# Performance work log

Measured on AMD Instinct MI355X. Metric: run time of the kernel, lower is better.

## Reference

```python
import jax, jax.numpy as jnp
import numpy as np

ALPHA = 0.2          # LeakyReLU negative slope
NEG_INF = -9e15      # mask value from the torch code
B, N, F, E, H, S, T, L = 32, 128, 78, 12, 256, 20, 13, 3


def setup_inputs() -> dict:
    key = jax.random.key(0)
    ks = jax.random.split(key, 20)
    sc = 0.05  # param scale
    inp = {
        "node_features": jax.random.normal(ks[0], (B, N, F), jnp.float32),
        "edge_features": jax.random.normal(ks[1], (B, N, N, E), jnp.float32),
        "adj_matrix": jax.random.randint(ks[2], (B, N, N), 0, 2).astype(jnp.int32),
        "scaffold_features": jax.random.normal(ks[3], (B, S), jnp.float32),
        # node projection (Linear F->H, with bias)
        "W_node": jax.random.normal(ks[4], (F, H), jnp.float32) * sc,
        "b_node": jnp.zeros((H,), jnp.float32),
        # stacked GAT layer params: W (H->H, no bias), a (2H->1, no bias)
        "gat_W": jax.random.normal(ks[5], (L, H, H), jnp.float32) * sc,
        "gat_a": jax.random.normal(ks[6], (L, 2 * H), jnp.float32) * sc,
        # scaffold projection (S->H)
        "W_sc": jax.random.normal(ks[7], (S, H), jnp.float32) * sc,
        "b_sc": jnp.zeros((H,), jnp.float32),
        # graph_pooling MLP: H -> H/2 -> H/4 (shared for graph + scaffold paths)
        "gp_w1": jax.random.normal(ks[8], (H, H // 2), jnp.float32) * sc,
        "gp_b1": jnp.zeros((H // 2,), jnp.float32),
        "gp_w2": jax.random.normal(ks[9], (H // 2, H // 4), jnp.float32) * sc,
        "gp_b2": jnp.zeros((H // 4,), jnp.float32),
        # output MLP: (H/4 + H/4) -> H/2 -> T
        "out_w1": jax.random.normal(ks[10], (H // 2, H // 2), jnp.float32) * sc,
        "out_b1": jnp.zeros((H // 2,), jnp.float32),
        "out_w2": jax.random.normal(ks[11], (H // 2, T), jnp.float32) * sc,
        "out_b2": jnp.zeros((T,), jnp.float32),
    }
    return inp


def _gat_stack(x, adj_matrix, gat_W, gat_a):
    # x: (B,N,H); adj: (B,N,N) int
    mask = adj_matrix > 0
    n_layers, _, h_dim = gat_W.shape
    for l in range(n_layers):
        h = jnp.einsum("bnf,fh->bnh", x, gat_W[l])      # (B,N,H)
        a1, a2 = gat_a[l, :h_dim], gat_a[l, h_dim:]
        # a . [h_i ; h_j] == h_i.a1 + h_j.a2 (exact decomposition of the
        # O(N^2, 2H) concat in the torch code)
        s1 = h @ a1                                       # (B,N)
        s2 = h @ a2                                       # (B,N)
        e = jax.nn.leaky_relu(s1[:, :, None] + s2[:, None, :], ALPHA)
        att = jnp.where(mask, e, NEG_INF)                 # (B,N,N)
        att = jax.nn.softmax(att, axis=-1)
        h_prime = jnp.einsum("bij,bjh->bih", att, h)
        x = jax.nn.relu(h_prime)                          # relu after layer (dropout = identity, eval)
    return x


def _pool(z, gp_w1, gp_b1, gp_w2, gp_b2):
    z = jax.nn.relu(z @ gp_w1 + gp_b1)
    return jax.nn.relu(z @ gp_w2 + gp_b2)


def reference(node_features, edge_features, adj_matrix, scaffold_features,
              W_node, b_node, gat_W, gat_a, W_sc, b_sc,
              gp_w1, gp_b1, gp_w2, gp_b2, out_w1, out_b1, out_w2, out_b2):
    # edge_features is accepted but unused in the original forward
    x = node_features @ W_node + b_node                  # (B,N,H)
    x = _gat_stack(x, adj_matrix, gat_W, gat_a)
    graph = x.mean(axis=1)                               # (B,H)
    g = _pool(graph, gp_w1, gp_b1, gp_w2, gp_b2)         # (B,H/4)
    s = _pool(scaffold_features @ W_sc + b_sc, gp_w1, gp_b1, gp_w2, gp_b2)
    c = jnp.concatenate([g, s], axis=-1)                 # (B,H/2)
    hdn = jax.nn.relu(c @ out_w1 + out_b1)
    return hdn @ out_w2 + out_b2                         # (B,T)
```

## Files before the change

kernel.cpp:

```cpp
#include <hip/hip_runtime.h>
#include <hip/hip_bf16.h>

#define NEG_INF -9.0e15f

using u16 = unsigned short;

__device__ __forceinline__ float b2f(__hip_bfloat16 v) { return __bfloat162float(v); }
__device__ __forceinline__ float ldv(const float* p, int i) { return p[i]; }
__device__ __forceinline__ float ldv(const __hip_bfloat16* p, int i) { return __bfloat162float(p[i]); }

__device__ __forceinline__ void async16(const void* g, void* l) {
    __builtin_amdgcn_global_load_lds(
        (__attribute__((address_space(1))) void*)(g),
        (__attribute__((address_space(3))) void*)(l), 16, 0, 0);
}

__device__ __forceinline__ int sniff(const void* wnode) {
    const u16* w = (const u16*)wnode;
    int lane = threadIdx.x & 63;
    u16 u = w[2 * lane];
    int e = (u >> 7) & 0xFF;
    unsigned long long m = __ballot(e >= 100 && e <= 140);
    return __popcll(m) >= 48;
}

__global__ __launch_bounds__(256) void k_gat(
    const float* __restrict__ x, const void* __restrict__ gat_W,
    const void* __restrict__ gat_a, int layer,
    const void* __restrict__ nf, const void* __restrict__ Wn_raw,
    const void* __restrict__ bn, int first,
    float* __restrict__ h, float* __restrict__ s1, float* __restrict__ s2) {
    __shared__ float xsT[256 * 10];
    __shared__ u16 Wbuf[2][32 * 256];
    const int t = threadIdx.x;
    const int bx = blockIdx.x;
    const int row0 = bx * 8;
    const int tx = t & 63, w = t >> 6;
    const int isbf = sniff(Wn_raw);
    const int c0 = 4 * tx;

    float acc0[4], acc1[4];

    if (isbf) {
        const u16* Wl = (const u16*)gat_W + (size_t)layer * 65536;

        auto stage_rows = [&](const u16* src, int r0, int nr, int b) {
            const char* g = (const char*)src + (size_t)r0 * 512;
            char* l = (char*)&Wbuf[b][0];
            int bytes = nr * 512;
            for (int off = t * 16; off < bytes; off += 4096)
                async16(g + off, l + off);
        };
        auto tile_compute = [&](int b, int k0, int nr) {
            const u16* Wb = &Wbuf[b][0];
            #pragma unroll 8
            for (int kk = 0; kk < nr; ++kk) {
                uint2 wv = *(const uint2*)(Wb + kk * 256 + c0);
                float w0 = __uint_as_float(wv.x << 16);
                float w1 = __uint_as_float(wv.x & 0xffff0000u);
                float w2 = __uint_as_float(wv.y << 16);
                float w3 = __uint_as_float(wv.y & 0xffff0000u);
                float2 xp = *(const float2*)&xsT[(k0 + kk) * 10 + 2 * w];
                acc0[0] += xp.x * w0; acc0[1] += xp.x * w1;
                acc0[2] += xp.x * w2; acc0[3] += xp.x * w3;
                acc1[0] += xp.y * w0; acc1[1] += xp.y * w1;
                acc1[2] += xp.y * w2; acc1[3] += xp.y * w3;
            }
        };

        int pb;
        if (first) {
            const u16* Wnl = (const u16*)Wn_raw;
            stage_rows(Wnl, 0, 32, 0);
            const u16* nfu = (const u16*)nf;
            for (int i = t; i < 624; i += 256) {
                int r = i / 78, k = i - r * 78;
                xsT[k * 10 + r] = __uint_as_float(((unsigned)nfu[(row0 + r) * 78 + k]) << 16);
            }
            const __hip_bfloat16* bnb = (const __hip_bfloat16*)bn;
            #pragma unroll
            for (int j = 0; j < 4; ++j) { acc0[j] = b2f(bnb[c0 + j]); acc1[j] = acc0[j]; }
            __syncthreads();
            stage_rows(Wnl, 32, 32, 1);
            tile_compute(0, 0, 32);
            __syncthreads();
            stage_rows(Wnl, 64, 14, 0);
            tile_compute(1, 32, 32);
            __syncthreads();
            stage_rows(Wl, 0, 32, 1);
            tile_compute(0, 64, 14);
            __syncthreads();
            #pragma unroll
            for (int j = 0; j < 4; ++j) {
                xsT[(c0 + j) * 10 + 2 * w]     = acc0[j];
                xsT[(c0 + j) * 10 + 2 * w + 1] = acc1[j];
            }
            __syncthreads();
            pb = 1;
        } else {
            stage_rows(Wl, 0, 32, 0);
            int r = t >> 5, cb = (t & 31) * 8;
            const float4* xp = (const float4*)(x + (size_t)(row0 + r) * 256 + cb);
            float4 f0 = xp[0], f1 = xp[1];
            xsT[(cb + 0) * 10 + r] = f0.x; xsT[(cb + 1) * 10 + r] = f0.y;
            xsT[(cb + 2) * 10 + r] = f0.z; xsT[(cb + 3) * 10 + r] = f0.w;
            xsT[(cb + 4) * 10 + r] = f1.x; xsT[(cb + 5) * 10 + r] = f1.y;
            xsT[(cb + 6) * 10 + r] = f1.z; xsT[(cb + 7) * 10 + r] = f1.w;
            __syncthreads();
            pb = 0;
        }
        #pragma unroll
        for (int j = 0; j < 4; ++j) { acc0[j] = 0.f; acc1[j] = 0.f; }
        for (int tt = 0; tt < 8; ++tt) {
            if (tt < 7) stage_rows(Wl, 32 * (tt + 1), 32, pb ^ 1);
            tile_compute(pb, 32 * tt, 32);
            __syncthreads();
            pb ^= 1;
        }
        const __hip_bfloat16* ga = (const __hip_bfloat16*)gat_a + (size_t)layer * 512;
        float d10 = 0.f, d20 = 0.f, d11 = 0.f, d21 = 0.f;
        #pragma unroll
        for (int j = 0; j < 4; ++j) {
            float a1v = b2f(ga[c0 + j]), a2v = b2f(ga[256 + c0 + j]);
            d10 += acc0[j] * a1v; d20 += acc0[j] * a2v;
            d11 += acc1[j] * a1v; d21 += acc1[j] * a2v;
        }
        #pragma unroll
        for (int off = 1; off < 64; off <<= 1) {
            d10 += __shfl_xor(d10, off, 64); d20 += __shfl_xor(d20, off, 64);
            d11 += __shfl_xor(d11, off, 64); d21 += __shfl_xor(d21, off, 64);
        }
        if (tx == 0) {
            s1[row0 + 2 * w] = d10;     s2[row0 + 2 * w] = d20;
            s1[row0 + 2 * w + 1] = d11; s2[row0 + 2 * w + 1] = d21;
        }
        *(float4*)&h[(size_t)(row0 + 2 * w) * 256 + c0]     = (float4){acc0[0], acc0[1], acc0[2], acc0[3]};
        *(float4*)&h[(size_t)(row0 + 2 * w + 1) * 256 + c0] = (float4){acc1[0], acc1[1], acc1[2], acc1[3]};
    } else {
        const float* Wlf = (const float*)gat_W + (size_t)layer * 65536;
        const float* gaf = (const float*)gat_a + (size_t)layer * 512;
        if (first) {
            const float* nff = (const float*)nf;
            for (int i = t; i < 624; i += 256) {
                int r = i / 78, k = i - r * 78;
                xsT[k * 10 + r] = nff[(row0 + r) * 78 + k];
            }
            __syncthreads();
            const float* Wnf = (const float*)Wn_raw;
            const float* bnf = (const float*)bn;
            #pragma unroll
            for (int j = 0; j < 4; ++j) { acc0[j] = bnf[c0 + j]; acc1[j] = acc0[j]; }
            for (int k = 0; k < 78; ++k) {
                float4 wf = *(const float4*)(Wnf + k * 256 + c0);
                float2 xp = *(const float2*)&xsT[k * 10 + 2 * w];
                acc0[0] += xp.x * wf.x; acc0[1] += xp.x * wf.y;
                acc0[2] += xp.x * wf.z; acc0[3] += xp.x * wf.w;
                acc1[0] += xp.y * wf.x; acc1[1] += xp.y * wf.y;
                acc1[2] += xp.y * wf.z; acc1[3] += xp.y * wf.w;
            }
            __syncthreads();
            #pragma unroll
            for (int j = 0; j < 4; ++j) {
                xsT[(c0 + j) * 10 + 2 * w]     = acc0[j];
                xsT[(c0 + j) * 10 + 2 * w + 1] = acc1[j];
            }
            __syncthreads();
        } else {
            int r = t >> 5, cb = (t & 31) * 8;
            const float4* xp = (const float4*)(x + (size_t)(row0 + r) * 256 + cb);
            float4 f0 = xp[0], f1 = xp[1];
            xsT[(cb + 0) * 10 + r] = f0.x; xsT[(cb + 1) * 10 + r] = f0.y;
            xsT[(cb + 2) * 10 + r] = f0.z; xsT[(cb + 3) * 10 + r] = f0.w;
            xsT[(cb + 4) * 10 + r] = f1.x; xsT[(cb + 5) * 10 + r] = f1.y;
            xsT[(cb + 6) * 10 + r] = f1.z; xsT[(cb + 7) * 10 + r] = f1.w;
            __syncthreads();
        }
        #pragma unroll
        for (int j = 0; j < 4; ++j) { acc0[j] = 0.f; acc1[j] = 0.f; }
        #pragma unroll 4
        for (int k = 0; k < 256; ++k) {
            float4 wf = *(const float4*)(Wlf + k * 256 + c0);
            float2 xp = *(const float2*)&xsT[k * 10 + 2 * w];
            acc0[0] += xp.x * wf.x; acc0[1] += xp.x * wf.y;
            acc0[2] += xp.x * wf.z; acc0[3] += xp.x * wf.w;
            acc1[0] += xp.y * wf.x; acc1[1] += xp.y * wf.y;
            acc1[2] += xp.y * wf.z; acc1[3] += xp.y * wf.w;
        }
        float d10 = 0.f, d20 = 0.f, d11 = 0.f, d21 = 0.f;
        #pragma unroll
        for (int j = 0; j < 4; ++j) {
            float a1v = gaf[c0 + j], a2v = gaf[256 + c0 + j];
            d10 += acc0[j] * a1v; d20 += acc0[j] * a2v;
            d11 += acc1[j] * a1v; d21 += acc1[j] * a2v;
        }
        #pragma unroll
        for (int off = 1; off < 64; off <<= 1) {
            d10 += __shfl_xor(d10, off, 64); d20 += __shfl_xor(d20, off, 64);
            d11 += __shfl_xor(d11, off, 64); d21 += __shfl_xor(d21, off, 64);
        }
        if (tx == 0) {
            s1[row0 + 2 * w] = d10;     s2[row0 + 2 * w] = d20;
            s1[row0 + 2 * w + 1] = d11; s2[row0 + 2 * w + 1] = d21;
        }
        *(float4*)&h[(size_t)(row0 + 2 * w) * 256 + c0]     = (float4){acc0[0], acc0[1], acc0[2], acc0[3]};
        *(float4*)&h[(size_t)(row0 + 2 * w + 1) * 256 + c0] = (float4){acc1[0], acc1[1], acc1[2], acc1[3]};
    }
}

__global__ __launch_bounds__(256) void k_attn(
    const float* __restrict__ h, const float* __restrict__ s1,
    const float* __restrict__ s2, const int* __restrict__ adj,
    float* __restrict__ x, float* __restrict__ gpart, int do_pool) {
    __shared__ float att_t[128][10];
    __shared__ __align__(16) float hbuf[2][32 * 256];
    __shared__ float pool_red[4][256];
    int blk = blockIdx.x, b = blk >> 4, i0 = (blk & 15) << 3;
    int t = threadIdx.x, w = t >> 6, lane = t & 63;
    const char* hbytes = (const char*)(h + (size_t)b * 32768);
    const int ph = blk & 3;
    {
        char* lb = (char*)&hbuf[0][0];
        const char* g = hbytes + ph * 32768;
        #pragma unroll
        for (int i = 0; i < 8; ++i)
            async16(g + i * 4096 + t * 16, lb + i * 4096 + t * 16);
    }
    {
        int cc0 = lane, cc1 = lane + 64;
        int ir0 = i0 + 2 * w, ir1 = ir0 + 1;
        const int* a0 = adj + (size_t)(b * 128 + ir0) * 128;
        const int* a1 = adj + (size_t)(b * 128 + ir1) * 128;
        int m00 = a0[cc0], m01 = a0[cc1], m10 = a1[cc0], m11 = a1[cc1];
        float sv0 = s1[b * 128 + ir0], sv1 = s1[b * 128 + ir1];
        float t0 = s2[b * 128 + cc0],  t1 = s2[b * 128 + cc1];
        float e00 = sv0 + t0; e00 = (e00 >= 0.f) ? e00 : 0.2f * e00;
        float e01 = sv0 + t1; e01 = (e01 >= 0.f) ? e01 : 0.2f * e01;
        float e10 = sv1 + t0; e10 = (e10 >= 0.f) ? e10 : 0.2f * e10;
        float e11 = sv1 + t1; e11 = (e11 >= 0.f) ? e11 : 0.2f * e11;
        float v00 = (m00 > 0) ? e00 : NEG_INF;
        float v01 = (m01 > 0) ? e01 : NEG_INF;
        float v10 = (m10 > 0) ? e10 : NEG_INF;
        float v11 = (m11 > 0) ? e11 : NEG_INF;
        float mx0 = fmaxf(v00, v01), mx1 = fmaxf(v10, v11);
        #pragma unroll
        for (int off = 1; off < 64; off <<= 1) {
            mx0 = fmaxf(mx0, __shfl_xor(mx0, off, 64));
            mx1 = fmaxf(mx1, __shfl_xor(mx1, off, 64));
        }
        float p00 = __expf(v00 - mx0), p01 = __expf(v01 - mx0);
        float p10 = __expf(v10 - mx1), p11 = __expf(v11 - mx1);
        float s0 = p00 + p01, ss1 = p10 + p11;
        #pragma unroll
        for (int off = 1; off < 64; off <<= 1) {
            s0  += __shfl_xor(s0, off, 64);
            ss1 += __shfl_xor(ss1, off, 64);
        }
        float inv0 = 1.0f / s0, inv1 = 1.0f / ss1;
        att_t[cc0][2 * w]     = p00 * inv0;
        att_t[cc1][2 * w]     = p01 * inv0;
        att_t[cc0][2 * w + 1] = p10 * inv1;
        att_t[cc1][2 * w + 1] = p11 * inv1;
    }
    __syncthreads();
    int tx = t & 63, ty = t >> 6;
    float acc0[4] = {0.f, 0.f, 0.f, 0.f}, acc1[4] = {0.f, 0.f, 0.f, 0.f};
    for (int c = 0; c < 4; ++c) {
        if (c < 3) {
            char* lb = (char*)&hbuf[(c + 1) & 1][0];
            const char* g = hbytes + (((c + 1 + ph) & 3) * 32768);
            #pragma unroll
            for (int i = 0; i < 8; ++i)
                async16(g + i * 4096 + t * 16, lb + i * 4096 + t * 16);
        }
        const float* hc = &hbuf[c & 1][0];
        const int jb = ((c + ph) & 3) * 32;
        #pragma unroll 4
        for (int jj = 0; jj < 32; ++jj) {
            float4 hv = *(const float4*)&hc[jj * 256 + 4 * tx];
            float2 ap = *(const float2*)&att_t[jb + jj][2 * ty];
            acc0[0] += ap.x * hv.x; acc0[1] += ap.x * hv.y;
            acc0[2] += ap.x * hv.z; acc0[3] += ap.x * hv.w;
            acc1[0] += ap.y * hv.x; acc1[1] += ap.y * hv.y;
            acc1[2] += ap.y * hv.z; acc1[3] += ap.y * hv.w;
        }
        __syncthreads();
    }
    if (!do_pool) {
        float4 o0 = {fmaxf(acc0[0],0.f), fmaxf(acc0[1],0.f), fmaxf(acc0[2],0.f), fmaxf(acc0[3],0.f)};
        float4 o1 = {fmaxf(acc1[0],0.f), fmaxf(acc1[1],0.f), fmaxf(acc1[2],0.f), fmaxf(acc1[3],0.f)};
        *(float4*)&x[(size_t)(b * 128 + i0 + 2 * ty)     * 256 + 4 * tx] = o0;
        *(float4*)&x[(size_t)(b * 128 + i0 + 2 * ty + 1) * 256 + 4 * tx] = o1;
    } else {
        float4 pr = {(fmaxf(acc0[0],0.f) + fmaxf(acc1[0],0.f)) * (1.f/128.f),
                     (fmaxf(acc0[1],0.f) + fmaxf(acc1[1],0.f)) * (1.f/128.f),
                     (fmaxf(acc0[2],0.f) + fmaxf(acc1[2],0.f)) * (1.f/128.f),
                     (fmaxf(acc0[3],0.f) + fmaxf(acc1[3],0.f)) * (1.f/128.f)};
        *(float4*)&pool_red[ty][4 * tx] = pr;
        __syncthreads();
        if (t < 64) {
            float4 r0 = ((const float4*)&pool_red[0][0])[t];
            float4 r1 = ((const float4*)&pool_red[1][0])[t];
            float4 r2 = ((const float4*)&pool_red[2][0])[t];
            float4 r3 = ((const float4*)&pool_red[3][0])[t];
            float4 o = {r0.x+r1.x+r2.x+r3.x, r0.y+r1.y+r2.y+r3.y,
                        r0.z+r1.z+r2.z+r3.z, r0.w+r1.w+r2.w+r3.w};
            *(float4*)&gpart[((size_t)b * 16 + (blk & 15)) * 256 + 4 * t] = o;
        }
    }
}

template <typename T>
__device__ __forceinline__ void head_body(
    int b, int t, const float* __restrict__ gpart,
    const T* scaf, const T* W_sc, const T* b_sc,
    const T* gp_w1, const T* gp_b1, const T* gp_w2, const T* gp_b2,
    const T* out_w1, const T* out_b1, const T* out_w2, const T* out_b2,
    float* gin_s, float* sproj, float* scaf_s,
    float* red1, float* red2, float* z1g, float* z1s,
    float* cvec, float* hdn, float* outv) {
    float g = 0.f;
    #pragma unroll
    for (int gg = 0; gg < 16; ++gg) g += gpart[((size_t)b * 16 + gg) * 256 + t];
    gin_s[t] = g;
    if (t < 20) scaf_s[t] = ldv(scaf, b * 20 + t);
    __syncthreads();
    {
        float sa = ldv(b_sc, t);
        #pragma unroll
        for (int k = 0; k < 20; ++k) sa += scaf_s[k] * ldv(W_sc, k * 256 + t);
        sproj[t] = sa;
    }
    __syncthreads();
    {
        int j = t & 127, khalf = t >> 7;
        int k0 = khalf * 128;
        float a1 = 0.f, a2 = 0.f;
        #pragma unroll 16
        for (int kk = 0; kk < 128; ++kk) {
            int k = k0 + kk;
            float wv = ldv(gp_w1, k * 128 + j);
            a1 += gin_s[k] * wv;
            a2 += sproj[k] * wv;
        }
        red1[t] = a1; red2[t] = a2;
    }
    __syncthreads();
    if (t < 128) {
        float bb = ldv(gp_b1, t);
        z1g[t] = fmaxf(bb + red1[t] + red1[t + 128], 0.f);
        z1s[t] = fmaxf(bb + red2[t] + red2[t + 128], 0.f);
    }
    __syncthreads();
    {
        int j = t & 63, q = t >> 6;
        int k0 = q * 32;
        float a1 = 0.f, a2 = 0.f;
        #pragma unroll
        for (int kk = 0; kk < 32; ++kk) {
            int k = k0 + kk;
            float wv = ldv(gp_w2, k * 64 + j);
            a1 += z1g[k] * wv;
            a2 += z1s[k] * wv;
        }
        red1[t] = a1; red2[t] = a2;
    }
    __syncthreads();
    if (t < 64) {
        float bb = ldv(gp_b2, t);
        cvec[t]      = fmaxf(bb + red1[t] + red1[t + 64] + red1[t + 128] + red1[t + 192], 0.f);
        cvec[64 + t] = fmaxf(bb + red2[t] + red2[t + 64] + red2[t + 128] + red2[t + 192], 0.f);
    }
    __syncthreads();
    {
        int j = t & 127, khalf = t >> 7;
        int k0 = khalf * 64;
        float a = 0.f;
        #pragma unroll 16
        for (int kk = 0; kk < 64; ++kk) {
            int k = k0 + kk;
            a += cvec[k] * ldv(out_w1, k * 128 + j);
        }
        red1[t] = a;
    }
    __syncthreads();
    if (t < 128) hdn[t] = fmaxf(ldv(out_b1, t) + red1[t] + red1[t + 128], 0.f);
    __syncthreads();
    if (t < 13) {
        float a = ldv(out_b2, t);
        #pragma unroll 16
        for (int k = 0; k < 128; ++k) a += hdn[k] * ldv(out_w2, k * 13 + t);
        outv[t] = a;
    }
}

__global__ __launch_bounds__(256) void k_head(
    const float* __restrict__ gpart, const void* __restrict__ scaf,
    const void* __restrict__ W_sc, const void* __restrict__ b_sc,
    const void* __restrict__ gp_w1, const void* __restrict__ gp_b1,
    const void* __restrict__ gp_w2, const void* __restrict__ gp_b2,
    const void* __restrict__ out_w1, const void* __restrict__ out_b1,
    const void* __restrict__ out_w2, const void* __restrict__ out_b2,
    void* __restrict__ out, const void* __restrict__ Wn) {
    int isbf = sniff(Wn);
    int b = blockIdx.x;
    int t = threadIdx.x;
    __shared__ float gin_s[256], sproj[256], scaf_s[20];
    __shared__ float red1[256], red2[256];
    __shared__ float z1g[128], z1s[128], cvec[128], hdn[128], outv[13];
    if (isbf) {
        head_body<__hip_bfloat16>(b, t, gpart,
            (const __hip_bfloat16*)scaf, (const __hip_bfloat16*)W_sc, (const __hip_bfloat16*)b_sc,
            (const __hip_bfloat16*)gp_w1, (const __hip_bfloat16*)gp_b1,
            (const __hip_bfloat16*)gp_w2, (const __hip_bfloat16*)gp_b2,
            (const __hip_bfloat16*)out_w1, (const __hip_bfloat16*)out_b1,
            (const __hip_bfloat16*)out_w2, (const __hip_bfloat16*)out_b2,
            gin_s, sproj, scaf_s, red1, red2, z1g, z1s, cvec, hdn, outv);
    } else {
        head_body<float>(b, t, gpart,
            (const float*)scaf, (const float*)W_sc, (const float*)b_sc,
            (const float*)gp_w1, (const float*)gp_b1,
            (const float*)gp_w2, (const float*)gp_b2,
            (const float*)out_w1, (const float*)out_b1,
            (const float*)out_w2, (const float*)out_b2,
            gin_s, sproj, scaf_s, red1, red2, z1g, z1s, cvec, hdn, outv);
    }
    __syncthreads();
    if (t < 13) {
        if (isbf) ((__hip_bfloat16*)out)[b * 13 + t] = __float2bfloat16(outv[t]);
        else      ((float*)out)[b * 13 + t] = outv[t];
    }
}

extern "C" void kernel_launch(void* const* d_in, const int* in_sizes, int n_in,
                              void* d_out, int out_size, void* d_ws, size_t ws_size,
                              hipStream_t stream) {
    (void)in_sizes; (void)n_in; (void)out_size; (void)ws_size;
    const void* nf     = d_in[0];
    const int*  adj    = (const int*)d_in[2];
    const void* scaf   = d_in[3];
    const void* W_node = d_in[4];
    const void* b_node = d_in[5];
    const void* gat_W  = d_in[6];
    const void* gat_a  = d_in[7];
    const void* W_sc   = d_in[8];
    const void* b_sc   = d_in[9];
    const void* gp_w1  = d_in[10];
    const void* gp_b1  = d_in[11];
    const void* gp_w2  = d_in[12];
    const void* gp_b2  = d_in[13];
    const void* out_w1 = d_in[14];
    const void* out_b1 = d_in[15];
    const void* out_w2 = d_in[16];
    const void* out_b2 = d_in[17];

    float* ws    = (float*)d_ws;
    float* x     = ws;
    float* h     = ws + 1048576;
    float* s1    = ws + 2097152;
    float* s2    = s1 + 4096;
    float* gpart = s2 + 4096;

    for (int l = 0; l < 3; ++l) {
        k_gat<<<512, 256, 0, stream>>>(x, gat_W, gat_a, l,
                                       nf, W_node, b_node, (l == 0) ? 1 : 0,
                                       h, s1, s2);
        k_attn<<<512, 256, 0, stream>>>(h, s1, s2, adj, x, gpart, (l == 2) ? 1 : 0);
    }
    k_head<<<32, 256, 0, stream>>>(gpart, scaf, W_sc, b_sc, gp_w1, gp_b1, gp_w2, gp_b2,
                                   out_w1, out_b1, out_w2, out_b2, d_out, W_node);
}
```

Baseline: 223.9 us.

## Fuse GAT layers, attention and head into one cooperative persistent kernel

Replaces the seven separate kernel launches (three projection, three attention, one head) with a single cooperative kernel that uses grid-wide syncs between stages. The h and s1/s2 buffers are double-buffered so one layer's attention reads cannot collide with the next layer's writes. Blocks are remapped so each block produces the same x rows it later consumes, which avoids one grid sync per layer. This targets launch gaps and per-kernel ramp-up, at the cost of grid-barrier latency and of only 32 blocks doing work in the head stage. A fallback to the old multi-launch path is kept in case the cooperative launch fails.

```diff
diff --git a/kernel.cpp b/kernel.cpp
--- a/kernel.cpp
+++ b/kernel.cpp
@@ -1,8 +1,10 @@
 #include <hip/hip_runtime.h>
 #include <hip/hip_bf16.h>
+#include <hip/hip_cooperative_groups.h>
 
 #define NEG_INF -9.0e15f
 
+namespace cg = cooperative_groups;
 using u16 = unsigned short;
 
 __device__ __forceinline__ float b2f(__hip_bfloat16 v) { return __bfloat162float(v); }
@@ -24,38 +26,35 @@
     return __popcll(m) >= 48;
 }
 
-__global__ __launch_bounds__(256) void k_gat(
+
+template <int IS_BF>
+__device__ __forceinline__ void gat_body(
+    char* smem, int t, int row0, int l, int first,
     const float* __restrict__ x, const void* __restrict__ gat_W,
-    const void* __restrict__ gat_a, int layer,
+    const void* __restrict__ gat_a,
     const void* __restrict__ nf, const void* __restrict__ Wn_raw,
-    const void* __restrict__ bn, int first,
-    float* __restrict__ h, float* __restrict__ s1, float* __restrict__ s2) {
-    __shared__ float xsT[256 * 10];
-    __shared__ u16 Wbuf[2][32 * 256];
-    const int t = threadIdx.x;
-    const int bx = blockIdx.x;
-    const int row0 = bx * 8;
+    const void* __restrict__ bn,
+    float* __restrict__ hw, float* __restrict__ s1w, float* __restrict__ s2w) {
+    float* xsT = (float*)smem;
     const int tx = t & 63, w = t >> 6;
-    const int isbf = sniff(Wn_raw);
     const int c0 = 4 * tx;
-
     float acc0[4], acc1[4];
 
-    if (isbf) {
-        const u16* Wl = (const u16*)gat_W + (size_t)layer * 65536;
-
-        auto stage_rows = [&](const u16* src, int r0, int nr, int b) {
+    if (IS_BF) {
+        u16* Wb0 = (u16*)(smem + 10240);
+        const u16* Wl = (const u16*)gat_W + (size_t)l * 65536;
+        auto stage_rows = [&](const u16* src, int r0, int nr, int buf) {
             const char* g = (const char*)src + (size_t)r0 * 512;
-            char* l = (char*)&Wbuf[b][0];
+            char* lp = (char*)(Wb0 + buf * 8192);
             int bytes = nr * 512;
             for (int off = t * 16; off < bytes; off += 4096)
-                async16(g + off, l + off);
+                async16(g + off, lp + off);
         };
-        auto tile_compute = [&](int b, int k0, int nr) {
-            const u16* Wb = &Wbuf[b][0];
+        auto tile_compute = [&](int buf, int k0, int nr) {
+            const u16* Wp = Wb0 + buf * 8192;
             #pragma unroll 8
             for (int kk = 0; kk < nr; ++kk) {
-                uint2 wv = *(const uint2*)(Wb + kk * 256 + c0);
+                uint2 wv = *(const uint2*)(Wp + kk * 256 + c0);
                 float w0 = __uint_as_float(wv.x << 16);
                 float w1 = __uint_as_float(wv.x & 0xffff0000u);
                 float w2 = __uint_as_float(wv.y << 16);
@@ -67,7 +66,6 @@
                 acc1[2] += xp.y * w2; acc1[3] += xp.y * w3;
             }
         };
-
         int pb;
         if (first) {
             const u16* Wnl = (const u16*)Wn_raw;
@@ -117,7 +115,7 @@
             __syncthreads();
             pb ^= 1;
         }
-        const __hip_bfloat16* ga = (const __hip_bfloat16*)gat_a + (size_t)layer * 512;
+        const __hip_bfloat16* ga = (const __hip_bfloat16*)gat_a + (size_t)l * 512;
         float d10 = 0.f, d20 = 0.f, d11 = 0.f, d21 = 0.f;
         #pragma unroll
         for (int j = 0; j < 4; ++j) {
@@ -131,14 +129,14 @@
             d11 += __shfl_xor(d11, off, 64); d21 += __shfl_xor(d21, off, 64);
         }
         if (tx == 0) {
-            s1[row0 + 2 * w] = d10;     s2[row0 + 2 * w] = d20;
-            s1[row0 + 2 * w + 1] = d11; s2[row0 + 2 * w + 1] = d21;
-        }
-        *(float4*)&h[(size_t)(row0 + 2 * w) * 256 + c0]     = (float4){acc0[0], acc0[1], acc0[2], acc0[3]};
-        *(float4*)&h[(size_t)(row0 + 2 * w + 1) * 256 + c0] = (float4){acc1[0], acc1[1], acc1[2], acc1[3]};
+            s1w[row0 + 2 * w] = d10;     s2w[row0 + 2 * w] = d20;
+            s1w[row0 + 2 * w + 1] = d11; s2w[row0 + 2 * w + 1] = d21;
+        }
+        *(float4*)&hw[(size_t)(row0 + 2 * w) * 256 + c0]     = (float4){acc0[0], acc0[1], acc0[2], acc0[3]};
+        *(float4*)&hw[(size_t)(row0 + 2 * w + 1) * 256 + c0] = (float4){acc1[0], acc1[1], acc1[2], acc1[3]};
     } else {
-        const float* Wlf = (const float*)gat_W + (size_t)layer * 65536;
-        const float* gaf = (const float*)gat_a + (size_t)layer * 512;
+        const float* Wlf = (const float*)gat_W + (size_t)l * 65536;
+        const float* gaf = (const float*)gat_a + (size_t)l * 512;
         if (first) {
             const float* nff = (const float*)nf;
             for (int i = t; i < 624; i += 256) {
@@ -199,27 +197,28 @@
             d11 += __shfl_xor(d11, off, 64); d21 += __shfl_xor(d21, off, 64);
         }
         if (tx == 0) {
-            s1[row0 + 2 * w] = d10;     s2[row0 + 2 * w] = d20;
-            s1[row0 + 2 * w + 1] = d11; s2[row0 + 2 * w + 1] = d21;
-        }
-        *(float4*)&h[(size_t)(row0 + 2 * w) * 256 + c0]     = (float4){acc0[0], acc0[1], acc0[2], acc0[3]};
-        *(float4*)&h[(size_t)(row0 + 2 * w + 1) * 256 + c0] = (float4){acc1[0], acc1[1], acc1[2], acc1[3]};
-    }
-}
-
-__global__ __launch_bounds__(256) void k_attn(
-    const float* __restrict__ h, const float* __restrict__ s1,
-    const float* __restrict__ s2, const int* __restrict__ adj,
+            s1w[row0 + 2 * w] = d10;     s2w[row0 + 2 * w] = d20;
+            s1w[row0 + 2 * w + 1] = d11; s2w[row0 + 2 * w + 1] = d21;
+        }
+        *(float4*)&hw[(size_t)(row0 + 2 * w) * 256 + c0]     = (float4){acc0[0], acc0[1], acc0[2], acc0[3]};
+        *(float4*)&hw[(size_t)(row0 + 2 * w + 1) * 256 + c0] = (float4){acc1[0], acc1[1], acc1[2], acc1[3]};
+    }
+}
+
+__device__ __forceinline__ void attn_body(
+    char* smem, int t, int b, int s,
+    const float* __restrict__ hw, const float* __restrict__ s1w,
+    const float* __restrict__ s2w, const int* __restrict__ adj,
     float* __restrict__ x, float* __restrict__ gpart, int do_pool) {
-    __shared__ float att_t[128][10];
-    __shared__ __align__(16) float hbuf[2][32 * 256];
-    __shared__ float pool_red[4][256];
-    int blk = blockIdx.x, b = blk >> 4, i0 = (blk & 15) << 3;
-    int t = threadIdx.x, w = t >> 6, lane = t & 63;
-    const char* hbytes = (const char*)(h + (size_t)b * 32768);
-    const int ph = blk & 3;
+    float (*att_t)[10] = (float (*)[10])smem;
+    float* hbuf = (float*)(smem + 5120);
+    float (*pool_red)[256] = (float (*)[256])(smem + 70656);
+    const int i0 = s << 3;
+    const int w = t >> 6, lane = t & 63;
+    const char* hbytes = (const char*)(hw + (size_t)b * 32768);
+    const int ph = s & 3;
     {
-        char* lb = (char*)&hbuf[0][0];
+        char* lb = (char*)hbuf;
         const char* g = hbytes + ph * 32768;
         #pragma unroll
         for (int i = 0; i < 8; ++i)
@@ -231,8 +230,8 @@
         const int* a0 = adj + (size_t)(b * 128 + ir0) * 128;
         const int* a1 = adj + (size_t)(b * 128 + ir1) * 128;
         int m00 = a0[cc0], m01 = a0[cc1], m10 = a1[cc0], m11 = a1[cc1];
-        float sv0 = s1[b * 128 + ir0], sv1 = s1[b * 128 + ir1];
-        float t0 = s2[b * 128 + cc0],  t1 = s2[b * 128 + cc1];
+        float sv0 = s1w[b * 128 + ir0], sv1 = s1w[b * 128 + ir1];
+        float t0 = s2w[b * 128 + cc0],  t1 = s2w[b * 128 + cc1];
         float e00 = sv0 + t0; e00 = (e00 >= 0.f) ? e00 : 0.2f * e00;
         float e01 = sv0 + t1; e01 = (e01 >= 0.f) ? e01 : 0.2f * e01;
         float e10 = sv1 + t0; e10 = (e10 >= 0.f) ? e10 : 0.2f * e10;
@@ -249,13 +248,13 @@
         }
         float p00 = __expf(v00 - mx0), p01 = __expf(v01 - mx0);
         float p10 = __expf(v10 - mx1), p11 = __expf(v11 - mx1);
-        float s0 = p00 + p01, ss1 = p10 + p11;
+        float sm0 = p00 + p01, sm1 = p10 + p11;
         #pragma unroll
         for (int off = 1; off < 64; off <<= 1) {
-            s0  += __shfl_xor(s0, off, 64);
-            ss1 += __shfl_xor(ss1, off, 64);
-        }
-        float inv0 = 1.0f / s0, inv1 = 1.0f / ss1;
+            sm0 += __shfl_xor(sm0, off, 64);
+            sm1 += __shfl_xor(sm1, off, 64);
+        }
+        float inv0 = 1.0f / sm0, inv1 = 1.0f / sm1;
         att_t[cc0][2 * w]     = p00 * inv0;
         att_t[cc1][2 * w]     = p01 * inv0;
         att_t[cc0][2 * w + 1] = p10 * inv1;
@@ -263,38 +262,39 @@
     }
     __syncthreads();
     int tx = t & 63, ty = t >> 6;
-    float acc0[4] = {0.f, 0.f, 0.f, 0.f}, acc1[4] = {0.f, 0.f, 0.f, 0.f};
+    float ac0[4] = {0.f, 0.f, 0.f, 0.f}, ac1[4] = {0.f, 0.f, 0.f, 0.f};
     for (int c = 0; c < 4; ++c) {
         if (c < 3) {
-            char* lb = (char*)&hbuf[(c + 1) & 1][0];
+            char* lb = (char*)hbuf + ((c + 1) & 1) * 32768;
             const char* g = hbytes + (((c + 1 + ph) & 3) * 32768);
             #pragma unroll
             for (int i = 0; i < 8; ++i)
                 async16(g + i * 4096 + t * 16, lb + i * 4096 + t * 16);
         }
-        const float* hc = &hbuf[c & 1][0];
+        const float* hc = hbuf + (c & 1) * 8192;
         const int jb = ((c + ph) & 3) * 32;
         #pragma unroll 4
         for (int jj = 0; jj < 32; ++jj) {
             float4 hv = *(const float4*)&hc[jj * 256 + 4 * tx];
             float2 ap = *(const float2*)&att_t[jb + jj][2 * ty];
-            acc0[0] += ap.x * hv.x; acc0[1] += ap.x * hv.y;
-            acc0[2] += ap.x * hv.z; acc0[3] += ap.x * hv.w;
-            acc1[0] += ap.y * hv.x; acc1[1] += ap.y * hv.y;
-            acc1[2] += ap.y * hv.z; acc1[3] += ap.y * hv.w;
+            ac0[0] += ap.x * hv.x; ac0[1] += ap.x * hv.y;
+            ac0[2] += ap.x * hv.z; ac0[3] += ap.x * hv.w;
+            ac1[0] += ap.y * hv.x; ac1[1] += ap.y * hv.y;
+            ac1[2] += ap.y * hv.z; ac1[3] += ap.y * hv.w;
         }
         __syncthreads();
     }
     if (!do_pool) {
-        float4 o0 = {fmaxf(acc0[0],0.f), fmaxf(acc0[1],0.f), fmaxf(acc0[2],0.f), fmaxf(acc0[3],0.f)};
-        float4 o1 = {fmaxf(acc1[0],0.f), fmaxf(acc1[1],0.f), fmaxf(acc1[2],0.f), fmaxf(acc1[3],0.f)};
+        float4 o0 = {fmaxf(ac0[0],0.f), fmaxf(ac0[1],0.f), fmaxf(ac0[2],0.f), fmaxf(ac0[3],0.f)};
+        float4 o1 = {fmaxf(ac1[0],0.f), fmaxf(ac1[1],0.f), fmaxf(ac1[2],0.f), fmaxf(ac1[3],0.f)};
         *(float4*)&x[(size_t)(b * 128 + i0 + 2 * ty)     * 256 + 4 * tx] = o0;
         *(float4*)&x[(size_t)(b * 128 + i0 + 2 * ty + 1) * 256 + 4 * tx] = o1;
+        __syncthreads();
     } else {
-        float4 pr = {(fmaxf(acc0[0],0.f) + fmaxf(acc1[0],0.f)) * (1.f/128.f),
-                     (fmaxf(acc0[1],0.f) + fmaxf(acc1[1],0.f)) * (1.f/128.f),
-                     (fmaxf(acc0[2],0.f) + fmaxf(acc1[2],0.f)) * (1.f/128.f),
-                     (fmaxf(acc0[3],0.f) + fmaxf(acc1[3],0.f)) * (1.f/128.f)};
+        float4 pr = {(fmaxf(ac0[0],0.f) + fmaxf(ac1[0],0.f)) * (1.f/128.f),
+                     (fmaxf(ac0[1],0.f) + fmaxf(ac1[1],0.f)) * (1.f/128.f),
+                     (fmaxf(ac0[2],0.f) + fmaxf(ac1[2],0.f)) * (1.f/128.f),
+                     (fmaxf(ac0[3],0.f) + fmaxf(ac1[3],0.f)) * (1.f/128.f)};
         *(float4*)&pool_red[ty][4 * tx] = pr;
         __syncthreads();
         if (t < 64) {
@@ -304,8 +304,9 @@
             float4 r3 = ((const float4*)&pool_red[3][0])[t];
             float4 o = {r0.x+r1.x+r2.x+r3.x, r0.y+r1.y+r2.y+r3.y,
                         r0.z+r1.z+r2.z+r3.z, r0.w+r1.w+r2.w+r3.w};
-            *(float4*)&gpart[((size_t)b * 16 + (blk & 15)) * 256 + 4 * t] = o;
-        }
+            *(float4*)&gpart[((size_t)b * 16 + s) * 256 + 4 * t] = o;
+        }
+        __syncthreads();
     }
 }
 
@@ -393,20 +394,22 @@
     }
 }
 
-__global__ __launch_bounds__(256) void k_head(
-    const float* __restrict__ gpart, const void* __restrict__ scaf,
-    const void* __restrict__ W_sc, const void* __restrict__ b_sc,
-    const void* __restrict__ gp_w1, const void* __restrict__ gp_b1,
-    const void* __restrict__ gp_w2, const void* __restrict__ gp_b2,
-    const void* __restrict__ out_w1, const void* __restrict__ out_b1,
-    const void* __restrict__ out_w2, const void* __restrict__ out_b2,
-    void* __restrict__ out, const void* __restrict__ Wn) {
-    int isbf = sniff(Wn);
-    int b = blockIdx.x;
-    int t = threadIdx.x;
-    __shared__ float gin_s[256], sproj[256], scaf_s[20];
-    __shared__ float red1[256], red2[256];
-    __shared__ float z1g[128], z1s[128], cvec[128], hdn[128], outv[13];
+__device__ __forceinline__ void head_dispatch(
+    char* smem, int isbf, int b, int t, const float* gpart,
+    const void* scaf, const void* W_sc, const void* b_sc,
+    const void* gp_w1, const void* gp_b1, const void* gp_w2, const void* gp_b2,
+    const void* out_w1, const void* out_b1, const void* out_w2, const void* out_b2,
+    void* out) {
+    float* gin_s = (float*)smem;
+    float* sproj = (float*)(smem + 1024);
+    float* red1  = (float*)(smem + 2048);
+    float* red2  = (float*)(smem + 3072);
+    float* z1g   = (float*)(smem + 4096);
+    float* z1s   = (float*)(smem + 4608);
+    float* cvec  = (float*)(smem + 5120);
+    float* hdn   = (float*)(smem + 5632);
+    float* outv  = (float*)(smem + 6144);
+    float* scaf_s= (float*)(smem + 6208);
     if (isbf) {
         head_body<__hip_bfloat16>(b, t, gpart,
             (const __hip_bfloat16*)scaf, (const __hip_bfloat16*)W_sc, (const __hip_bfloat16*)b_sc,
@@ -429,6 +432,95 @@
         if (isbf) ((__hip_bfloat16*)out)[b * 13 + t] = __float2bfloat16(outv[t]);
         else      ((float*)out)[b * 13 + t] = outv[t];
     }
+}
+
+__global__ __launch_bounds__(256, 2) void k_fused(
+    const void* __restrict__ nf, const void* __restrict__ Wn_raw,
+    const void* __restrict__ bn,
+    const void* __restrict__ gat_W, const void* __restrict__ gat_a,
+    const int* __restrict__ adj,
+    float* __restrict__ x,
+    float* __restrict__ hA, float* __restrict__ hB,
+    float* __restrict__ s1A, float* __restrict__ s1B,
+    float* __restrict__ s2A, float* __restrict__ s2B,
+    float* __restrict__ gpart,
+    const void* __restrict__ scaf,
+    const void* __restrict__ W_sc, const void* __restrict__ b_sc,
+    const void* __restrict__ gp_w1, const void* __restrict__ gp_b1,
+    const void* __restrict__ gp_w2, const void* __restrict__ gp_b2,
+    const void* __restrict__ out_w1, const void* __restrict__ out_b1,
+    const void* __restrict__ out_w2, const void* __restrict__ out_b2,
+    void* __restrict__ out) {
+    __shared__ __align__(16) char smem[74752];
+    cg::grid_group grid = cg::this_grid();
+    const int t = threadIdx.x;
+    const int blk = blockIdx.x;
+    const int b = blk & 31;
+    const int s = blk >> 5;
+    const int row0 = b * 128 + s * 8;
+    const int isbf = sniff(Wn_raw);
+
+    for (int l = 0; l < 3; ++l) {
+        float* hw  = (l & 1) ? hB : hA;
+        float* s1w = (l & 1) ? s1B : s1A;
+        float* s2w = (l & 1) ? s2B : s2A;
+        if (isbf)
+            gat_body<1>(smem, t, row0, l, l == 0, x, gat_W, gat_a, nf, Wn_raw, bn, hw, s1w, s2w);
+        else
+            gat_body<0>(smem, t, row0, l, l == 0, x, gat_W, gat_a, nf, Wn_raw, bn, hw, s1w, s2w);
+
+        __syncthreads();
+        __threadfence();
+        grid.sync();
+        __threadfence();
+
+        attn_body(smem, t, b, s, hw, s1w, s2w, adj, x, gpart, (l == 2) ? 1 : 0);
+    }
+
+    __threadfence();
+    grid.sync();
+    __threadfence();
+    if (blk < 32)
+        head_dispatch(smem, isbf, blk, t, gpart, scaf, W_sc, b_sc,
+                      gp_w1, gp_b1, gp_w2, gp_b2,
+                      out_w1, out_b1, out_w2, out_b2, out);
+}
+
+__global__ __launch_bounds__(256) void k_gat(
+    const float* __restrict__ x, const void* __restrict__ gat_W,
+    const void* __restrict__ gat_a, int layer,
+    const void* __restrict__ nf, const void* __restrict__ Wn_raw,
+    const void* __restrict__ bn, int first,
+    float* __restrict__ h, float* __restrict__ s1, float* __restrict__ s2) {
+    __shared__ __align__(16) char smem[43008];
+    const int t = threadIdx.x;
+    const int row0 = blockIdx.x * 8;
+    if (sniff(Wn_raw))
+        gat_body<1>(smem, t, row0, layer, first, x, gat_W, gat_a, nf, Wn_raw, bn, h, s1, s2);
+    else
+        gat_body<0>(smem, t, row0, layer, first, x, gat_W, gat_a, nf, Wn_raw, bn, h, s1, s2);
+}
+
+__global__ __launch_bounds__(256) void k_attn(
+    const float* __restrict__ h, const float* __restrict__ s1,
+    const float* __restrict__ s2, const int* __restrict__ adj,
+    float* __restrict__ x, float* __restrict__ gpart, int do_pool) {
+    __shared__ __align__(16) char smem[74752];
+    int blk = blockIdx.x, b = blk >> 4, s = blk & 15;
+    attn_body(smem, threadIdx.x, b, s, h, s1, s2, adj, x, gpart, do_pool);
+}
+
+__global__ __launch_bounds__(256) void k_head(
+    const float* __restrict__ gpart, const void* __restrict__ scaf,
+    const void* __restrict__ W_sc, const void* __restrict__ b_sc,
+    const void* __restrict__ gp_w1, const void* __restrict__ gp_b1,
+    const void* __restrict__ gp_w2, const void* __restrict__ gp_b2,
+    const void* __restrict__ out_w1, const void* __restrict__ out_b1,
+    const void* __restrict__ out_w2, const void* __restrict__ out_b2,
+    void* __restrict__ out, const void* __restrict__ Wn) {
+    __shared__ __align__(16) char smem[8192];
+    head_dispatch(smem, sniff(Wn), blockIdx.x, threadIdx.x, gpart, scaf, W_sc, b_sc,
+                  gp_w1, gp_b1, gp_w2, gp_b2, out_w1, out_b1, out_w2, out_b2, out);
 }
 
 extern "C" void kernel_launch(void* const* d_in, const int* in_sizes, int n_in,
@@ -455,17 +547,35 @@
 
     float* ws    = (float*)d_ws;
     float* x     = ws;
-    float* h     = ws + 1048576;
-    float* s1    = ws + 2097152;
-    float* s2    = s1 + 4096;
-    float* gpart = s2 + 4096;
-
-    for (int l = 0; l < 3; ++l) {
-        k_gat<<<512, 256, 0, stream>>>(x, gat_W, gat_a, l,
-                                       nf, W_node, b_node, (l == 0) ? 1 : 0,
-                                       h, s1, s2);
-        k_attn<<<512, 256, 0, stream>>>(h, s1, s2, adj, x, gpart, (l == 2) ? 1 : 0);
-    }
-    k_head<<<32, 256, 0, stream>>>(gpart, scaf, W_sc, b_sc, gp_w1, gp_b1, gp_w2, gp_b2,
-                                   out_w1, out_b1, out_w2, out_b2, d_out, W_node);
-}
+    float* hA    = ws + 1048576;
+    float* hB    = ws + 2097152;
+    float* s1A   = ws + 3145728;
+    float* s2A   = ws + 3149824;
+    float* s1B   = ws + 3153920;
+    float* s2B   = ws + 3158016;
+    float* gpart = ws + 3162112;
+    void* out    = d_out;
+
+    void* args[] = {
+        (void*)&nf, (void*)&W_node, (void*)&b_node, (void*)&gat_W, (void*)&gat_a,
+        (void*)&adj, (void*)&x, (void*)&hA, (void*)&hB,
+        (void*)&s1A, (void*)&s1B, (void*)&s2A, (void*)&s2B, (void*)&gpart,
+        (void*)&scaf, (void*)&W_sc, (void*)&b_sc,
+        (void*)&gp_w1, (void*)&gp_b1, (void*)&gp_w2, (void*)&gp_b2,
+        (void*)&out_w1, (void*)&out_b1, (void*)&out_w2, (void*)&out_b2,
+        (void*)&out
+    };
+    hipError_t e = hipLaunchCooperativeKernel((const void*)k_fused, dim3(512), dim3(256),
+                                              args, 0, stream);
+    if (e != hipSuccess) {
+        (void)hipGetLastError();
+        for (int l = 0; l < 3; ++l) {
+            k_gat<<<512, 256, 0, stream>>>(x, gat_W, gat_a, l,
+                                           nf, W_node, b_node, (l == 0) ? 1 : 0,
+                                           hA, s1A, s2A);
+            k_attn<<<512, 256, 0, stream>>>(hA, s1A, s2A, adj, x, gpart, (l == 2) ? 1 : 0);
+        }
+        k_head<<<32, 256, 0, stream>>>(gpart, scaf, W_sc, b_sc, gp_w1, gp_b1, gp_w2, gp_b2,
+                                       out_w1, out_b1, out_w2, out_b2, d_out, W_node);
+    }
+}
```

New measurement: 894.8 us. 300% more time.
